# Kernel optimization log

Measured on AMD Instinct MI355X. Metric: run time of the kernel, lower is better.

Reference implementation:

```python
import jax, jax.numpy as jnp
import numpy as np

# db1 (Haar) filters, replicating the torch module's pywt-derived constants.
_s = np.float32(1.0 / np.sqrt(2.0))
_dl = np.array([_s, _s], np.float32)    # dec_lo[::-1]
_dh = np.array([_s, -_s], np.float32)   # dec_hi[::-1]
_rl = np.array([_s, _s], np.float32)    # rec_lo
_rh = np.array([_s, -_s], np.float32)   # rec_hi
# filters[k][i,j] = a[j]*b[i]  (torch: a.unsqueeze(0)*b.unsqueeze(1)) == outer(b, a)
DEC = jnp.asarray(np.stack([np.outer(_dl, _dl) / 2.0, np.outer(_dh, _dl), np.outer(_dl, _dh), np.outer(_dh, _dh)], 0))  # [4,2,2]
REC = jnp.asarray(np.stack([np.outer(_rl, _rl) * 2.0, np.outer(_rh, _rl), np.outer(_rl, _rh), np.outer(_rh, _rh)], 0))  # [4,2,2]


def wt(x):
    # stride-2 2x2 conv per channel == linear mix of 2x2 blocks; fused over all channels
    B, C, H, W = x.shape
    xb = x.reshape(B, C, H // 2, 2, W // 2, 2)
    y = jnp.einsum('kpq,bchpwq->bckhw', DEC, xb)  # [B,C,4,H/2,W/2]
    y = jnp.concatenate([y[:, :, :1], (y[:, :, 1:] + 1.0) * 0.5], axis=2)  # rescale HF bands
    return y.reshape(B, 4 * C, H // 2, W // 2)


def iwt(y):
    B, C4, H, W = y.shape
    C = C4 // 4
    yb = y.reshape(B, C, 4, H, W)
    yb = jnp.concatenate([yb[:, :, :1], 2.0 * yb[:, :, 1:] - 1.0], axis=2)  # undo HF rescale
    x = jnp.einsum('kpq,bckhw->bchpwq', REC, yb)  # conv_transpose2d, stride 2, no overlap
    return x.reshape(B, C, 2 * H, 2 * W)


def conv3x3(x, w, b):
    y = jax.lax.conv_general_dilated(x, w, (1, 1), ((1, 1), (1, 1)), dimension_numbers=('NCHW', 'OIHW', 'NCHW'))
    return y + b[None, :, None, None]


def setup_inputs() -> dict:
    key = jax.random.key(0)
    ks = jax.random.split(key, 20)
    B, Cin, H, W = 8, 1, 512, 512
    c = 16
    inp = {'x': jax.random.normal(ks[0], (B, Cin, H, W), jnp.float32)}
    specs = [('conv1', c, 4 * Cin), ('conv2', 4 * c, 4 * c), ('conv3', 16 * c, 16 * c), ('conv4', 64 * c, 64 * c),
             ('convd1', 4, c), ('convd2', c, 2 * c), ('convd3', 4 * c, 8 * c), ('convd4', 16 * c, 32 * c)]
    for idx, (name, o, i) in enumerate(specs):
        kw, kb = jax.random.split(ks[1 + idx])
        inp[name + '_w'] = jax.random.normal(kw, (o, i, 3, 3), jnp.float32) / np.float32(np.sqrt(i * 9))
        inp[name + '_b'] = jax.random.normal(kb, (o,), jnp.float32) * 0.01
    return inp


def reference(x, conv1_w, conv1_b, conv2_w, conv2_b, conv3_w, conv3_b, conv4_w, conv4_b,
              convd1_w, convd1_b, convd2_w, convd2_b, convd3_w, convd3_b, convd4_w, convd4_b):
    lrelu = lambda t: jax.nn.leaky_relu(t, 0.2)
    w1 = wt(x);  c1 = lrelu(conv3x3(w1, conv1_w, conv1_b))
    w2 = wt(c1); c2 = lrelu(conv3x3(w2, conv2_w, conv2_b))
    w3 = wt(c2); c3 = lrelu(conv3x3(w3, conv3_w, conv3_b))
    w4 = wt(c3); c4 = lrelu(conv3x3(w4, conv4_w, conv4_b))
    c5 = lrelu(conv3x3(c4, conv4_w, conv4_b))  # conv4 reused, as in the torch module
    c6 = conv3x3(c5, conv4_w, conv4_b)
    ic4 = lrelu(c6 + w4)
    ic3 = lrelu(conv3x3(jnp.concatenate([c3, iwt(ic4)], 1), convd4_w, convd4_b))
    ic2 = lrelu(conv3x3(jnp.concatenate([c2, iwt(ic3)], 1), convd3_w, convd3_b))
    ic1 = lrelu(conv3x3(jnp.concatenate([c1, iwt(ic2)], 1), convd2_w, convd2_b))
    iw1 = lrelu(conv3x3(ic1, convd1_w, convd1_b))
    logits = iwt(iw1)
    return jax.nn.sigmoid(logits)
```

## Files before the change

kernel.cpp:

```cpp
#include <hip/hip_runtime.h>
#include <cstddef>


typedef unsigned short u16;
typedef unsigned int u32;
typedef __bf16 bf16x8 __attribute__((ext_vector_type(8)));
typedef float floatx4 __attribute__((ext_vector_type(4)));
typedef u16 u16x4 __attribute__((ext_vector_type(4)));
typedef u16 u16x8 __attribute__((ext_vector_type(8)));

__device__ __forceinline__ float b2f(u16 h) {
    union { u32 u; float f; } x; x.u = ((u32)h) << 16; return x.f;
}
__device__ __forceinline__ u16 f2b(float f) {
    union { float f; u32 u; } x; x.f = f;
    return (u16)((x.u + 0x7FFFu + ((x.u >> 16) & 1u)) >> 16);
}
__device__ __forceinline__ float lrelu_f(float v) { return v > 0.f ? v : 0.2f * v; }

__device__ __forceinline__ void gld16(const u16* g, u16* l) {
    __builtin_amdgcn_global_load_lds(
        (const __attribute__((address_space(1))) u32*)(const void*)g,
        (__attribute__((address_space(3))) u32*)(void*)l, 16, 0, 0);
}

template<int NT>
__global__ __launch_bounds__(256)
void conv_mfma_k(const u16* __restrict__ in, int Cin, int iWp, int iImg,
                 const u16* __restrict__ wb, const float* __restrict__ bias,
                 const u16* __restrict__ skip, int sC, int sWp, int sImg, int spad,
                 u16* __restrict__ out, int Cst, int oWp, int oImg, int opad,
                 int logW, int logH)
{
    constexpr int BM = 128, BN = NT * 32;
    constexpr int ASZ = BM * 32;
    constexpr int BSZ = BN * 32;
    __shared__ u16 At[2 * ASZ];
    __shared__ u16 Bt[2 * BSZ];

    const int tid = threadIdx.x;
    const int wid = tid >> 6, lane = tid & 63;
    const int W = 1 << logW, H = 1 << logH;
    const int mBase = blockIdx.x * BM;
    const int nBase = blockIdx.y * BN;
    const int K = 9 * Cin;
    const int kg = lane & 3;
    const int rr = lane >> 2;
    const int kgs = kg ^ ((rr >> 1) & 3);

    const u16 *gA0, *gA1, *gB0, *gB1 = nullptr;
    {
        int m0 = mBase + wid * 32 + rr;
        int px0 = m0 & (W - 1), py0 = (m0 >> logW) & (H - 1), pb0 = m0 >> (logW + logH);
        gA0 = in + ((size_t)pb0 * iImg + (size_t)py0 * iWp + px0) * Cin + kgs * 8;
        int m1 = m0 + 16;
        int px1 = m1 & (W - 1), py1 = (m1 >> logW) & (H - 1), pb1 = m1 >> (logW + logH);
        gA1 = in + ((size_t)pb1 * iImg + (size_t)py1 * iWp + px1) * Cin + kgs * 8;
    }
    if constexpr (NT == 4) {
        gB0 = wb + (size_t)(nBase + wid * 32 + rr) * K + kgs * 8;
        gB1 = wb + (size_t)(nBase + wid * 32 + 16 + rr) * K + kgs * 8;
    } else {
        gB0 = wb + (size_t)(nBase + wid * 16 + rr) * K + kgs * 8;
    }
    u16* lA0 = &At[wid * 1024];
    u16* lA1 = &At[wid * 1024 + 512];
    u16* lB0 = (NT == 4) ? &Bt[wid * 1024] : &Bt[wid * 512];
    u16* lB1 = (NT == 4) ? &Bt[wid * 1024 + 512] : nullptr;

    const int wm = wid >> 1, wn = wid & 1;
    const int fm = lane & 15;
    const int fk = ((lane >> 4) * 8) ^ (((fm >> 1) & 3) << 3);

    floatx4 acc[4][NT] = {};

    const int nChunks = K / 32;
    const size_t rowStep = (size_t)(iWp - 2) * Cin;
    int cbn = 0, tap = 0;

    auto stage = [&](int buf) {
        gld16(gA0, lA0 + buf * ASZ);
        gld16(gA1, lA1 + buf * ASZ);
        gld16(gB0, lB0 + buf * BSZ);
        if constexpr (NT == 4) gld16(gB1, lB1 + buf * BSZ);
        size_t dA = 32;
        cbn += 32;
        if (cbn == Cin) { cbn = 0; ++tap; dA = ((tap % 3 == 0) ? rowStep : (size_t)Cin) - (size_t)(Cin - 32); }
        gA0 += dA; gA1 += dA;
        gB0 += 32;
        if constexpr (NT == 4) gB1 += 32;
    };

    auto compute = [&](int buf) {
        const u16* Ab = &At[buf * ASZ];
        const u16* Bb = &Bt[buf * BSZ];
        bf16x8 af[4], bfr[NT];
#pragma unroll
        for (int mt = 0; mt < 4; ++mt)
            af[mt] = *(const bf16x8*)&Ab[(wm * 64 + mt * 16 + fm) * 32 + fk];
#pragma unroll
        for (int nt = 0; nt < NT; ++nt)
            bfr[nt] = *(const bf16x8*)&Bb[(wn * (NT * 16) + nt * 16 + fm) * 32 + fk];
        __builtin_amdgcn_s_setprio(1);
#pragma unroll
        for (int mt = 0; mt < 4; ++mt)
#pragma unroll
            for (int nt = 0; nt < NT; ++nt)
                acc[mt][nt] = __builtin_amdgcn_mfma_f32_16x16x32_bf16(af[mt], bfr[nt], acc[mt][nt], 0, 0, 0);
        __builtin_amdgcn_s_setprio(0);
    };

    stage(0);
    __syncthreads();
    for (int kc = 0; kc < nChunks; kc += 2) {
        stage(1);
        compute(0);
        __syncthreads();
        if (kc + 2 < nChunks) stage(0);
        compute(1);
        __syncthreads();
    }

    const int rq = (lane >> 4) * 4;
#pragma unroll
    for (int mt = 0; mt < 4; ++mt) {
        const int mrow = mBase + wm * 64 + mt * 16 + rq;
#pragma unroll
        for (int r = 0; r < 4; ++r) {
            int m2 = mrow + r;
            int px = m2 & (W - 1), py = (m2 >> logW) & (H - 1), pb = m2 >> (logW + logH);
            size_t ob = ((size_t)pb * oImg + (size_t)(py + opad) * oWp + (px + opad)) * Cst;
            size_t sb = 0;
            if (skip) sb = ((size_t)pb * sImg + (size_t)(py + spad) * sWp + (px + spad)) * sC;
#pragma unroll
            for (int nt = 0; nt < NT; ++nt) {
                int n = nBase + wn * (NT * 16) + nt * 16 + fm;
                float v = acc[mt][nt][r] + bias[n];
                if (skip) v += b2f(skip[sb + n]);
                v = lrelu_f(v);
                out[ob + n] = f2b(v);
            }
        }
    }
}

__global__ __launch_bounds__(256)
void conv_n16_k(const u16* __restrict__ in, int iWp, int iImg,
                const u16* __restrict__ wb, const float* __restrict__ bias,
                u16* __restrict__ out, int logW, int logH)
{
    __shared__ u16 At[128 * 32];
    __shared__ u16 Bt[16 * 32];
    const int tid = threadIdx.x;
    const int wid = tid >> 6, lane = tid & 63;
    const int W = 1 << logW, H = 1 << logH;
    const int mBase = blockIdx.x * 128;
    const int kg = lane & 3, rr = lane >> 2;
    const int kgs = kg ^ ((rr >> 1) & 3);

    const u16 *gA0, *gA1;
    {
        int m0 = mBase + wid * 32 + rr;
        int px0 = m0 & (W - 1), py0 = (m0 >> logW) & (H - 1), pb0 = m0 >> (logW + logH);
        gA0 = in + ((size_t)pb0 * iImg + (size_t)py0 * iWp + px0) * 32 + kgs * 8;
        int m1 = m0 + 16;
        int px1 = m1 & (W - 1), py1 = (m1 >> logW) & (H - 1), pb1 = m1 >> (logW + logH);
        gA1 = in + ((size_t)pb1 * iImg + (size_t)py1 * iWp + px1) * 32 + kgs * 8;
    }
    const u16* gB = wb + (size_t)rr * 288 + kgs * 8;
    u16* lA0 = &At[wid * 1024];
    u16* lA1 = &At[wid * 1024 + 512];

    const int fm = lane & 15;
    const int fk = ((lane >> 4) * 8) ^ (((fm >> 1) & 3) << 3);
    floatx4 acc[2] = {};
    const size_t rowStep = (size_t)(iWp - 2) * 32;

    for (int tap = 0; tap < 9; ++tap) {
        gld16(gA0, lA0);
        gld16(gA1, lA1);
        if (wid == 0) gld16(gB, &Bt[0]);
        __syncthreads();
        bf16x8 bf = *(const bf16x8*)&Bt[fm * 32 + fk];
#pragma unroll
        for (int mt = 0; mt < 2; ++mt) {
            bf16x8 af = *(const bf16x8*)&At[(wid * 32 + mt * 16 + fm) * 32 + fk];
            acc[mt] = __builtin_amdgcn_mfma_f32_16x16x32_bf16(af, bf, acc[mt], 0, 0, 0);
        }
        __syncthreads();
        size_t dA = (tap % 3 == 2) ? rowStep : (size_t)32;
        gA0 += dA; gA1 += dA; gB += 32;
    }

    const int rq = (lane >> 4) * 4;
    const float bn = bias[fm];
#pragma unroll
    for (int mt = 0; mt < 2; ++mt) {
#pragma unroll
        for (int r = 0; r < 4; ++r) {
            int m2 = mBase + wid * 32 + mt * 16 + rq + r;
            out[(size_t)m2 * 16 + fm] = f2b(lrelu_f(acc[mt][r] + bn));
        }
    }
}

template<int CIN, int COUT>
__global__ __launch_bounds__(256)
void conv_direct_k(const u16* __restrict__ in, int Sin,
                   const float* __restrict__ w, const float* __restrict__ bias,
                   u16* __restrict__ out, int Sout, int oWp, int oImg, int opad,
                   int logW, int logH, int total)
{
    int m = blockIdx.x * 256 + threadIdx.x;
    if (m >= total) return;
    const int W = 1 << logW, H = 1 << logH;
    const int px = m & (W - 1);
    const int py = (m >> logW) & (H - 1);
    const int pb = m >> (logW + logH);
    float acc[COUT];
#pragma unroll
    for (int o = 0; o < COUT; ++o) acc[o] = bias[o];
    for (int tap = 0; tap < 9; ++tap) {
        int dy = tap / 3 - 1, dx = tap % 3 - 1;
        int iy = py + dy, ix = px + dx;
        if ((unsigned)iy >= (unsigned)H || (unsigned)ix >= (unsigned)W) continue;
        const u16* p = in + (size_t)((((pb << logH) + iy) << logW) + ix) * Sin;
        if constexpr (CIN == 4) {
            u16x4 v = *(const u16x4*)p;
#pragma unroll
            for (int ci = 0; ci < 4; ++ci) {
                float f = b2f(v[ci]);
#pragma unroll
                for (int o = 0; o < COUT; ++o) acc[o] += f * w[(o * CIN + ci) * 9 + tap];
            }
        } else {
#pragma unroll
            for (int c8 = 0; c8 < CIN / 8; ++c8) {
                u16x8 v = *(const u16x8*)(p + c8 * 8);
#pragma unroll
                for (int j = 0; j < 8; ++j) {
                    int ci = c8 * 8 + j;
                    float f = b2f(v[j]);
#pragma unroll
                    for (int o = 0; o < COUT; ++o) acc[o] += f * w[(o * CIN + ci) * 9 + tap];
                }
            }
        }
    }
    size_t ob = ((size_t)pb * oImg + (size_t)(py + opad) * oWp + (px + opad)) * Sout;
#pragma unroll
    for (int o = 0; o < COUT; ++o)
        out[ob + o] = f2b(lrelu_f(acc[o]));
}

__global__ __launch_bounds__(256)
void wt_in_k(const float* __restrict__ x, u16* __restrict__ out, int total)
{
    int idx = blockIdx.x * 256 + threadIdx.x;
    if (idx >= total) return;
    int wq = idx & 255, t = idx >> 8;
    int hq = t & 255, b = t >> 8;
    const float* p = x + ((size_t)b * 512 + 2 * hq) * 512 + 2 * wq;
    float a = p[0], bv = p[1], cv = p[512], d = p[513];
    u16x4 o = { f2b(0.25f * (a + bv + cv + d)),
                f2b(0.25f * (a + bv - cv - d) + 0.5f),
                f2b(0.25f * (a - bv + cv - d) + 0.5f),
                f2b(0.25f * (a - bv - cv + d) + 0.5f) };
    *(u16x4*)&out[(size_t)idx * 4] = o;
}

__global__ __launch_bounds__(256)
void wt_k(const u16* __restrict__ in, int Sin, int iWp, int iImg, int ipad,
          u16* __restrict__ out, int Sout, int oWp, int oImg, int opad,
          int logC, int logWo, int logHo, int total)
{
    int idx = blockIdx.x * 256 + threadIdx.x;
    if (idx >= total) return;
    const int C = 1 << logC, Wo = 1 << logWo, Ho = 1 << logHo;
    int c = idx & (C - 1); int t = idx >> logC;
    int wq = t & (Wo - 1); t >>= logWo;
    int hq = t & (Ho - 1); int b = t >> logHo;
    size_t p00 = ((size_t)b * iImg + (size_t)(2 * hq + ipad) * iWp + (2 * wq + ipad)) * Sin + c;
    float a  = b2f(in[p00]);
    float bv = b2f(in[p00 + Sin]);
    float cv = b2f(in[p00 + (size_t)iWp * Sin]);
    float d  = b2f(in[p00 + (size_t)iWp * Sin + Sin]);
    u16x4 o = { f2b(0.25f * (a + bv + cv + d)),
                f2b(0.25f * (a + bv - cv - d) + 0.5f),
                f2b(0.25f * (a - bv + cv - d) + 0.5f),
                f2b(0.25f * (a - bv - cv + d) + 0.5f) };
    *(u16x4*)&out[((size_t)b * oImg + (size_t)(hq + opad) * oWp + (wq + opad)) * Sout + 4 * c] = o;
}

__global__ __launch_bounds__(256)
void iwt_k(const u16* __restrict__ in, int Sin, int logC, int logW, int logH,
           u16* __restrict__ out, int Sout, int oWp, int oImg, int opad, int total)
{
    int idx = blockIdx.x * 256 + threadIdx.x;
    if (idx >= total) return;
    const int C = 1 << logC, W = 1 << logW;
    int c = idx & (C - 1); int t = idx >> logC;
    int wq = t & (W - 1); t >>= logW;
    int hq = t & ((1 << logH) - 1); int b = t >> logH;
    u16x4 v = *(const u16x4*)&in[(size_t)((((b << logH) + hq) << logW) + wq) * Sin + 4 * c];
    float y0 = b2f(v[0]);
    float y1 = 2.f * b2f(v[1]) - 1.f;
    float y2 = 2.f * b2f(v[2]) - 1.f;
    float y3 = 2.f * b2f(v[3]) - 1.f;
    float x00 = y0 + 0.5f * ( y1 + y2 + y3);
    float x01 = y0 + 0.5f * ( y1 - y2 - y3);
    float x10 = y0 + 0.5f * (-y1 + y2 - y3);
    float x11 = y0 + 0.5f * (-y1 - y2 + y3);
    size_t q = ((size_t)b * oImg + (size_t)(2 * hq + opad) * oWp + (2 * wq + opad)) * Sout + c;
    out[q] = f2b(x00);
    out[q + Sout] = f2b(x01);
    out[q + (size_t)oWp * Sout] = f2b(x10);
    out[q + (size_t)oWp * Sout + Sout] = f2b(x11);
}

__global__ __launch_bounds__(256)
void iwt_out_k(const u16* __restrict__ in, float* __restrict__ out, int total)
{
    int idx = blockIdx.x * 256 + threadIdx.x;
    if (idx >= total) return;
    int wq = idx & 255, t = idx >> 8;
    int hq = t & 255, b = t >> 8;
    u16x4 v = *(const u16x4*)&in[(size_t)idx * 4];
    float y0 = b2f(v[0]);
    float y1 = 2.f * b2f(v[1]) - 1.f;
    float y2 = 2.f * b2f(v[2]) - 1.f;
    float y3 = 2.f * b2f(v[3]) - 1.f;
    float x00 = y0 + 0.5f * ( y1 + y2 + y3);
    float x01 = y0 + 0.5f * ( y1 - y2 - y3);
    float x10 = y0 + 0.5f * (-y1 + y2 - y3);
    float x11 = y0 + 0.5f * (-y1 - y2 + y3);
    float* q = out + ((size_t)b * 512 + 2 * hq) * 512 + 2 * wq;
    q[0]   = 1.f / (1.f + __expf(-x00));
    q[1]   = 1.f / (1.f + __expf(-x01));
    q[512] = 1.f / (1.f + __expf(-x10));
    q[513] = 1.f / (1.f + __expf(-x11));
}

__global__ __launch_bounds__(256)
void prep_w_k(const float* __restrict__ src, u16* __restrict__ dst, int logCIN, int total)
{
    int idx = blockIdx.x * 256 + threadIdx.x;
    if (idx >= total) return;
    const int CIN = 1 << logCIN;
    int ci = idx & (CIN - 1);
    int q = idx >> logCIN;
    int tap = q % 9, o = q / 9;
    dst[idx] = f2b(src[((size_t)(o * CIN + ci)) * 9 + tap]);
}

__global__ __launch_bounds__(256)
void zb_k(u16* __restrict__ buf, int Wp, int Hp, int C, int total)
{
    int idx = blockIdx.x * 256 + threadIdx.x;
    if (idx >= total) return;
    int c8 = idx % (C / 8); int t = idx / (C / 8);
    int nbp = 2 * Wp + 2 * (Hp - 2);
    int p = t % nbp; int b = t / nbp;
    int y, x;
    if (p < Wp) { y = 0; x = p; }
    else if (p < 2 * Wp) { y = Hp - 1; x = p - Wp; }
    else { int q = p - 2 * Wp; y = 1 + (q >> 1); x = (q & 1) ? Wp - 1 : 0; }
    u16x8 z = {0, 0, 0, 0, 0, 0, 0, 0};
    *(u16x8*)&buf[((size_t)b * Hp * Wp + (size_t)y * Wp + x) * C + c8 * 8] = z;
}

extern "C" void kernel_launch(void* const* d_in, const int* in_sizes, int n_in,
                              void* d_out, int out_size, void* d_ws, size_t ws_size,
                              hipStream_t stream)
{
    const float* x   = (const float*)d_in[0];
    const float* c1w = (const float*)d_in[1];  const float* c1b = (const float*)d_in[2];
    const float* c2w = (const float*)d_in[3];  const float* c2b = (const float*)d_in[4];
    const float* c3w = (const float*)d_in[5];  const float* c3b = (const float*)d_in[6];
    const float* c4w = (const float*)d_in[7];  const float* c4b = (const float*)d_in[8];
    const float* d1w = (const float*)d_in[9];  const float* d1b = (const float*)d_in[10];
    const float* d2w = (const float*)d_in[11]; const float* d2b = (const float*)d_in[12];
    const float* d3w = (const float*)d_in[13]; const float* d3b = (const float*)d_in[14];
    const float* d4w = (const float*)d_in[15]; const float* d4b = (const float*)d_in[16];

    const size_t MiB = 1u << 20;
    char* base = (char*)d_ws;
    u16* c4wb = (u16*)base;
    u16* c3wb = c4wb + 9437184;
    u16* d4wb = c3wb + 589824;
    u16* d3wb = d4wb + 1179648;
    u16* c2wb = d3wb + 73728;
    u16* d2wb = c2wb + 36864;
    u16* CAT1p = (u16*)(base + 22  * MiB);
    u16* CAT2p = (u16*)(base + 55  * MiB);
    u16* CAT3p = (u16*)(base + 88  * MiB);
    u16* P1    = (u16*)(base + 123 * MiB);
    u16* P2    = (u16*)(base + 142 * MiB);
    u16* P3    = (u16*)(base + 161 * MiB);
    float* outp = (float*)d_out;

    u16* W2p = P1; u16* W4p = P1; u16* IC2 = P1;
    u16* W3p = P2; u16* C4p = P2; u16* IC4 = P2; u16* IC1 = P2;
    u16* W1  = P3; u16* C5p = P3; u16* IC3 = P3; u16* IW1 = P3;

    auto cdiv = [](int a, int b) { return (a + b - 1) / b; };
    auto prep = [&](const float* s, u16* d, int logCIN, int total) {
        prep_w_k<<<cdiv(total, 256), 256, 0, stream>>>(s, d, logCIN, total);
    };
    auto zb = [&](u16* buf, int Wp, int Hp, int C) {
        int total = 8 * (2 * Wp + 2 * (Hp - 2)) * (C / 8);
        zb_k<<<cdiv(total, 256), 256, 0, stream>>>(buf, Wp, Hp, C, total);
    };
    auto mfma = [&](const u16* in, int Cin, int iWp, int iImg,
                    const u16* w, const float* bi,
                    const u16* skip, int sC, int sWp, int sImg, int spad,
                    int Cout, u16* out, int Cst, int oWp, int oImg, int opad,
                    int logW, int logH) {
        int M = 8 << (logW + logH);
        if (Cout % 128 == 0) {
            dim3 g(M / 128, Cout / 128);
            conv_mfma_k<4><<<g, 256, 0, stream>>>(in, Cin, iWp, iImg, w, bi,
                                                  skip, sC, sWp, sImg, spad,
                                                  out, Cst, oWp, oImg, opad, logW, logH);
        } else {
            dim3 g(M / 128, Cout / 64);
            conv_mfma_k<2><<<g, 256, 0, stream>>>(in, Cin, iWp, iImg, w, bi,
                                                  skip, sC, sWp, sImg, spad,
                                                  out, Cst, oWp, oImg, opad, logW, logH);
        }
    };

    prep(c4w, c4wb, 10, 9437184);
    prep(c3w, c3wb, 8, 589824);
    prep(d4w, d4wb, 9, 1179648);
    prep(d3w, d3wb, 7, 73728);
    prep(c2w, c2wb, 6, 36864);
    prep(d2w, d2wb, 5, 4608);
    zb(CAT1p, 258, 258, 32);
    zb(W2p, 130, 130, 64);
    zb(W3p, 66, 66, 256);
    zb(CAT2p, 130, 130, 128);
    zb(CAT3p, 66, 66, 512);

    const int P256 = 8 * 256 * 256;
    const int T2M = 2097152;
    const int I258 = 258 * 258;

    wt_in_k<<<cdiv(P256, 256), 256, 0, stream>>>(x, W1, P256);
    conv_direct_k<4, 16><<<cdiv(P256, 256), 256, 0, stream>>>(
        W1, 4, c1w, c1b, CAT1p, 32, 258, I258, 1, 8, 8, P256);
    zb(C5p, 34, 34, 1024);
    wt_k<<<cdiv(T2M, 256), 256, 0, stream>>>(CAT1p, 32, 258, I258, 1,
                                             W2p, 64, 130, 16900, 1, 4, 7, 7, T2M);
    mfma(W2p, 64, 130, 16900, c2wb, c2b, nullptr, 0, 0, 0, 0,
         64, CAT2p, 128, 130, 16900, 1, 7, 7);
    zb(W4p, 34, 34, 1024);
    wt_k<<<cdiv(T2M, 256), 256, 0, stream>>>(CAT2p, 128, 130, 16900, 1,
                                             W3p, 256, 66, 4356, 1, 6, 6, 6, T2M);
    mfma(W3p, 256, 66, 4356, c3wb, c3b, nullptr, 0, 0, 0, 0,
         256, CAT3p, 512, 66, 4356, 1, 6, 6);
    zb(C4p, 34, 34, 1024);
    wt_k<<<cdiv(T2M, 256), 256, 0, stream>>>(CAT3p, 512, 66, 4356, 1,
                                             W4p, 1024, 34, 1156, 1, 8, 5, 5, T2M);
    mfma(W4p, 1024, 34, 1156, c4wb, c4b, nullptr, 0, 0, 0, 0,
         1024, C4p, 1024, 34, 1156, 1, 5, 5);
    mfma(C4p, 1024, 34, 1156, c4wb, c4b, nullptr, 0, 0, 0, 0,
         1024, C5p, 1024, 34, 1156, 1, 5, 5);
    mfma(C5p, 1024, 34, 1156, c4wb, c4b, W4p, 1024, 34, 1156, 1,
         1024, IC4, 1024, 32, 1024, 0, 5, 5);
    iwt_k<<<cdiv(T2M, 256), 256, 0, stream>>>(IC4, 1024, 8, 5, 5,
                                              CAT3p + 256, 512, 66, 4356, 1, T2M);
    mfma(CAT3p, 512, 66, 4356, d4wb, d4b, nullptr, 0, 0, 0, 0,
         256, IC3, 256, 64, 4096, 0, 6, 6);
    iwt_k<<<cdiv(T2M, 256), 256, 0, stream>>>(IC3, 256, 6, 6, 6,
                                              CAT2p + 64, 128, 130, 16900, 1, T2M);
    mfma(CAT2p, 128, 130, 16900, d3wb, d3b, nullptr, 0, 0, 0, 0,
         64, IC2, 64, 128, 16384, 0, 7, 7);
    iwt_k<<<cdiv(T2M, 256), 256, 0, stream>>>(IC2, 64, 4, 7, 7,
                                              CAT1p + 16, 32, 258, I258, 1, T2M);
    conv_n16_k<<<dim3(P256 / 128), 256, 0, stream>>>(CAT1p, 258, I258, d2wb, d2b, IC1, 8, 8);
    conv_direct_k<16, 4><<<cdiv(P256, 256), 256, 0, stream>>>(
        IC1, 16, d1w, d1b, IW1, 4, 256, 65536, 0, 8, 8, P256);
    iwt_out_k<<<cdiv(P256, 256), 256, 0, stream>>>(IW1, outp, P256);
}
```

Measured before the change: 1.034 ms.

## Load MFMA B fragments directly from pre-tiled weights, dropping B LDS staging

Weights are pre-permuted into a fragment-ordered tiled layout so each lane can read its MFMA B operand straight from global memory into registers with one 16-byte load per tile. The B shared-memory buffer and its async LDS copies are removed, and B fragments are double-buffered in registers. Block indices are also remapped so blocks sharing an M tile run adjacently across N, which should improve cache reuse of activations. The change trades LDS traffic and capacity for more global/L2 weight reads per wave, which may expose latency.

```diff
diff --git a/kernel.cpp b/kernel.cpp
--- a/kernel.cpp
+++ b/kernel.cpp
@@ -34,21 +34,24 @@
 {
     constexpr int BM = 128, BN = NT * 32;
     constexpr int ASZ = BM * 32;
-    constexpr int BSZ = BN * 32;
     __shared__ u16 At[2 * ASZ];
-    __shared__ u16 Bt[2 * BSZ];
 
     const int tid = threadIdx.x;
     const int wid = tid >> 6, lane = tid & 63;
     const int W = 1 << logW, H = 1 << logH;
-    const int mBase = blockIdx.x * BM;
-    const int nBase = blockIdx.y * BN;
+
+    const int id = blockIdx.x + gridDim.x * blockIdx.y;
+    const int by = id % gridDim.y;
+    const int bx = id / gridDim.y;
+    const int mBase = bx * BM;
+    const int nBase = by * BN;
+
     const int K = 9 * Cin;
     const int kg = lane & 3;
     const int rr = lane >> 2;
     const int kgs = kg ^ ((rr >> 1) & 3);
 
-    const u16 *gA0, *gA1, *gB0, *gB1 = nullptr;
+    const u16 *gA0, *gA1;
     {
         int m0 = mBase + wid * 32 + rr;
         int px0 = m0 & (W - 1), py0 = (m0 >> logW) & (H - 1), pb0 = m0 >> (logW + logH);
@@ -57,50 +60,45 @@
         int px1 = m1 & (W - 1), py1 = (m1 >> logW) & (H - 1), pb1 = m1 >> (logW + logH);
         gA1 = in + ((size_t)pb1 * iImg + (size_t)py1 * iWp + px1) * Cin + kgs * 8;
     }
-    if constexpr (NT == 4) {
-        gB0 = wb + (size_t)(nBase + wid * 32 + rr) * K + kgs * 8;
-        gB1 = wb + (size_t)(nBase + wid * 32 + 16 + rr) * K + kgs * 8;
-    } else {
-        gB0 = wb + (size_t)(nBase + wid * 16 + rr) * K + kgs * 8;
-    }
     u16* lA0 = &At[wid * 1024];
     u16* lA1 = &At[wid * 1024 + 512];
-    u16* lB0 = (NT == 4) ? &Bt[wid * 1024] : &Bt[wid * 512];
-    u16* lB1 = (NT == 4) ? &Bt[wid * 1024 + 512] : nullptr;
 
     const int wm = wid >> 1, wn = wid & 1;
     const int fm = lane & 15;
     const int fk = ((lane >> 4) * 8) ^ (((fm >> 1) & 3) << 3);
 
+    const int nG = gridDim.y * (NT * 2);
+    const size_t bStride = (size_t)nG * 512;
+    const u16* gBbase = wb + (size_t)((nBase >> 4) + wn * NT) * 512 + lane * 8;
+
     floatx4 acc[4][NT] = {};
 
     const int nChunks = K / 32;
     const size_t rowStep = (size_t)(iWp - 2) * Cin;
     int cbn = 0, tap = 0;
 
-    auto stage = [&](int buf) {
+    auto stageA = [&](int buf) {
         gld16(gA0, lA0 + buf * ASZ);
         gld16(gA1, lA1 + buf * ASZ);
-        gld16(gB0, lB0 + buf * BSZ);
-        if constexpr (NT == 4) gld16(gB1, lB1 + buf * BSZ);
         size_t dA = 32;
         cbn += 32;
         if (cbn == Cin) { cbn = 0; ++tap; dA = ((tap % 3 == 0) ? rowStep : (size_t)Cin) - (size_t)(Cin - 32); }
         gA0 += dA; gA1 += dA;
-        gB0 += 32;
-        if constexpr (NT == 4) gB1 += 32;
     };
 
-    auto compute = [&](int buf) {
+    auto loadB = [&](bf16x8 (&dst)[NT], int kc) {
+        const u16* p = gBbase + (size_t)kc * bStride;
+#pragma unroll
+        for (int nt = 0; nt < NT; ++nt)
+            dst[nt] = *(const bf16x8*)(p + nt * 512);
+    };
+
+    auto compute = [&](int buf, const bf16x8 (&bfr)[NT]) {
         const u16* Ab = &At[buf * ASZ];
-        const u16* Bb = &Bt[buf * BSZ];
-        bf16x8 af[4], bfr[NT];
+        bf16x8 af[4];
 #pragma unroll
         for (int mt = 0; mt < 4; ++mt)
             af[mt] = *(const bf16x8*)&Ab[(wm * 64 + mt * 16 + fm) * 32 + fk];
-#pragma unroll
-        for (int nt = 0; nt < NT; ++nt)
-            bfr[nt] = *(const bf16x8*)&Bb[(wn * (NT * 16) + nt * 16 + fm) * 32 + fk];
         __builtin_amdgcn_s_setprio(1);
 #pragma unroll
         for (int mt = 0; mt < 4; ++mt)
@@ -110,14 +108,16 @@
         __builtin_amdgcn_s_setprio(0);
     };
 
-    stage(0);
+    bf16x8 bC[NT], bN[NT];
+    stageA(0); loadB(bC, 0);
     __syncthreads();
     for (int kc = 0; kc < nChunks; kc += 2) {
-        stage(1);
-        compute(0);
+        stageA(1);
+        loadB(bN, kc + 1);
+        compute(0, bC);
         __syncthreads();
-        if (kc + 2 < nChunks) stage(0);
-        compute(1);
+        if (kc + 2 < nChunks) { stageA(0); loadB(bC, kc + 2); }
+        compute(1, bN);
         __syncthreads();
     }
 
@@ -354,6 +354,25 @@
 }
 
 __global__ __launch_bounds__(256)
+void prep_w_tiled_k(const float* __restrict__ src, u16* __restrict__ dst,
+                    int logCIN, int logNG, int total)
+{
+    int idx = blockIdx.x * 256 + threadIdx.x;
+    if (idx >= total) return;
+    const int CIN = 1 << logCIN;
+    int j = idx & 7;
+    int r = (idx >> 3) & 15;
+    int q = (idx >> 7) & 3;
+    int t = idx >> 9;
+    int g = t & ((1 << logNG) - 1);
+    int kc = t >> logNG;
+    int o = g * 16 + r;
+    int k = kc * 32 + q * 8 + j;
+    int tap = k >> logCIN, ci = k & (CIN - 1);
+    dst[idx] = f2b(src[((size_t)o * CIN + ci) * 9 + tap]);
+}
+
+__global__ __launch_bounds__(256)
 void zb_k(u16* __restrict__ buf, int Wp, int Hp, int C, int total)
 {
     int idx = blockIdx.x * 256 + threadIdx.x;
@@ -404,8 +423,8 @@
     u16* W1  = P3; u16* C5p = P3; u16* IC3 = P3; u16* IW1 = P3;
 
     auto cdiv = [](int a, int b) { return (a + b - 1) / b; };
-    auto prep = [&](const float* s, u16* d, int logCIN, int total) {
-        prep_w_k<<<cdiv(total, 256), 256, 0, stream>>>(s, d, logCIN, total);
+    auto prepT = [&](const float* s, u16* d, int logCIN, int logNG, int total) {
+        prep_w_tiled_k<<<cdiv(total, 256), 256, 0, stream>>>(s, d, logCIN, logNG, total);
     };
     auto zb = [&](u16* buf, int Wp, int Hp, int C) {
         int total = 8 * (2 * Wp + 2 * (Hp - 2)) * (C / 8);
@@ -430,12 +449,12 @@
         }
     };
 
-    prep(c4w, c4wb, 10, 9437184);
-    prep(c3w, c3wb, 8, 589824);
-    prep(d4w, d4wb, 9, 1179648);
-    prep(d3w, d3wb, 7, 73728);
-    prep(c2w, c2wb, 6, 36864);
-    prep(d2w, d2wb, 5, 4608);
+    prepT(c4w, c4wb, 10, 6, 9437184);
+    prepT(c3w, c3wb, 8, 4, 589824);
+    prepT(d4w, d4wb, 9, 4, 1179648);
+    prepT(d3w, d3wb, 7, 2, 73728);
+    prepT(c2w, c2wb, 6, 2, 36864);
+    prep_w_k<<<cdiv(4608, 256), 256, 0, stream>>>(d2w, d2wb, 5, 4608);
     zb(CAT1p, 258, 258, 32);
     zb(W2p, 130, 130, 64);
     zb(W3p, 66, 66, 256);
```

New measurement: 1.179 ms. +14.0%, slower.

## Triple-buffer MFMA conv LDS staging with partial vmcnt waits

Applied to the files above, without the earlier changes.

Replaces the double-buffered K-loop with a three-stage LDS ring, keeping two chunks of global-to-LDS loads in flight while one is computed. Each iteration ends with a hand-written s_waitcnt vmcnt(N) plus barrier that waits only for the oldest stage's loads instead of draining all outstanding loads. The goal is to hide global memory latency better. In exchange it uses 1.5x more shared memory per block, which may reduce occupancy, and the hard-coded vmcnt values must match the number of loads each stage issues.

```diff
diff --git a/kernel.cpp b/kernel.cpp
--- a/kernel.cpp
+++ b/kernel.cpp
@@ -35,8 +35,8 @@
     constexpr int BM = 128, BN = NT * 32;
     constexpr int ASZ = BM * 32;
     constexpr int BSZ = BN * 32;
-    __shared__ u16 At[2 * ASZ];
-    __shared__ u16 Bt[2 * BSZ];
+    __shared__ u16 At[3 * ASZ];
+    __shared__ u16 Bt[3 * BSZ];
 
     const int tid = threadIdx.x;
     const int wid = tid >> 6, lane = tid & 63;
@@ -110,15 +110,27 @@
         __builtin_amdgcn_s_setprio(0);
     };
 
+    auto waitbar = [&](bool partial) {
+        if (partial) {
+            if constexpr (NT == 4) asm volatile("s_waitcnt vmcnt(4)\ns_barrier" ::: "memory");
+            else                   asm volatile("s_waitcnt vmcnt(3)\ns_barrier" ::: "memory");
+        } else {
+            asm volatile("s_waitcnt vmcnt(0)\ns_barrier" ::: "memory");
+        }
+    };
+
     stage(0);
-    __syncthreads();
-    for (int kc = 0; kc < nChunks; kc += 2) {
-        stage(1);
-        compute(0);
-        __syncthreads();
-        if (kc + 2 < nChunks) stage(0);
-        compute(1);
-        __syncthreads();
+    stage(1);
+    waitbar(true);
+
+    int cb = 0, pb = 2;
+    for (int kc = 0; kc < nChunks; ++kc) {
+        bool pre = (kc + 2 < nChunks);
+        if (pre) stage(pb);
+        compute(cb);
+        waitbar(pre);
+        pb = cb;
+        cb = (cb == 2) ? 0 : cb + 1;
     }
 
     const int rq = (lane >> 4) * 4;
@@ -128,10 +140,10 @@
 #pragma unroll
         for (int r = 0; r < 4; ++r) {
             int m2 = mrow + r;
-            int px = m2 & (W - 1), py = (m2 >> logW) & (H - 1), pb = m2 >> (logW + logH);
-            size_t ob = ((size_t)pb * oImg + (size_t)(py + opad) * oWp + (px + opad)) * Cst;
+            int px = m2 & (W - 1), py = (m2 >> logW) & (H - 1), pb2 = m2 >> (logW + logH);
+            size_t ob = ((size_t)pb2 * oImg + (size_t)(py + opad) * oWp + (px + opad)) * Cst;
             size_t sb = 0;
-            if (skip) sb = ((size_t)pb * sImg + (size_t)(py + spad) * sWp + (px + spad)) * sC;
+            if (skip) sb = ((size_t)pb2 * sImg + (size_t)(py + spad) * sWp + (px + spad)) * sC;
 #pragma unroll
             for (int nt = 0; nt < NT; ++nt) {
                 int n = nBase + wn * (NT * 16) + nt * 16 + fm;
```

Measured after the change: 1.086 ms. 5.0% more time.

## Split K across two wave groups in 512-thread conv kernel with LDS reduction

Applied to the files above, without the earlier changes.

Adds a 512-thread conv kernel for Cout%128 layers. Two groups of four waves each handle half of the K reduction, using separate double-buffered LDS regions. At the end the partial accumulators are summed through LDS before the fused bias/skip/lrelu epilogue. The goal is more waves per 128x128 tile, to hide latency on the deep-K layers, especially conv4 at small spatial size. In exchange it costs extra LDS traffic and a sync for the reduction. It also assumes nChunks splits evenly into even halves.

```diff
diff --git a/kernel.cpp b/kernel.cpp
--- a/kernel.cpp
+++ b/kernel.cpp
@@ -24,7 +24,146 @@
         (__attribute__((address_space(3))) u32*)(void*)l, 16, 0, 0);
 }
 
-template<int NT>
+__global__ __launch_bounds__(512, 4)
+void conv_mfma8_k(const u16* __restrict__ in, int Cin, int iWp, int iImg,
+                  const u16* __restrict__ wb, const float* __restrict__ bias,
+                  const u16* __restrict__ skip, int sC, int sWp, int sImg, int spad,
+                  u16* __restrict__ out, int Cst, int oWp, int oImg, int opad,
+                  int logW, int logH)
+{
+    __shared__ alignas(16) u16 S[32768];
+
+    const int tid = threadIdx.x;
+    const int wid = tid >> 6, lane = tid & 63;
+    const int half = wid >> 2, wl = wid & 3;
+    const int W = 1 << logW, H = 1 << logH;
+    const int mBase = blockIdx.x * 128;
+    const int nBase = blockIdx.y * 128;
+    const int K = 9 * Cin;
+    const int nChunks = K / 32;
+    const int nC = nChunks >> 1;
+
+    const int kg = lane & 3;
+    const int rr = lane >> 2;
+    const int kgs = kg ^ ((rr >> 1) & 3);
+
+    const int k0 = half * nC * 32;
+    int tap = k0 / Cin;
+    int cbn = k0 - tap * Cin;
+
+    const u16 *gA0, *gA1, *gB0, *gB1;
+    {
+        int ty = tap / 3, tx = tap - ty * 3;
+        int m0 = mBase + wl * 32 + rr;
+        int px0 = m0 & (W - 1), py0 = (m0 >> logW) & (H - 1), pb0 = m0 >> (logW + logH);
+        gA0 = in + ((size_t)pb0 * iImg + (size_t)(py0 + ty) * iWp + (px0 + tx)) * Cin + cbn + kgs * 8;
+        int m1 = m0 + 16;
+        int px1 = m1 & (W - 1), py1 = (m1 >> logW) & (H - 1), pb1 = m1 >> (logW + logH);
+        gA1 = in + ((size_t)pb1 * iImg + (size_t)(py1 + ty) * iWp + (px1 + tx)) * Cin + cbn + kgs * 8;
+    }
+    gB0 = wb + (size_t)(nBase + wl * 32 + rr) * K + k0 + kgs * 8;
+    gB1 = wb + (size_t)(nBase + wl * 32 + 16 + rr) * K + k0 + kgs * 8;
+
+    u16* Sb = &S[half * 16384];
+    u16* lA0 = Sb + wl * 1024;
+    u16* lA1 = Sb + wl * 1024 + 512;
+    u16* lB0 = Sb + 8192 + wl * 1024;
+    u16* lB1 = Sb + 8192 + wl * 1024 + 512;
+
+    const int wm = wl >> 1, wn = wl & 1;
+    const int fm = lane & 15;
+    const int fk = ((lane >> 4) * 8) ^ (((fm >> 1) & 3) << 3);
+
+    floatx4 acc[4][4] = {};
+
+    const size_t rowStep = (size_t)(iWp - 2) * Cin;
+
+    auto stage = [&](int buf) {
+        gld16(gA0, lA0 + buf * 4096);
+        gld16(gA1, lA1 + buf * 4096);
+        gld16(gB0, lB0 + buf * 4096);
+        gld16(gB1, lB1 + buf * 4096);
+        size_t dA = 32;
+        cbn += 32;
+        if (cbn == Cin) { cbn = 0; ++tap; dA = ((tap % 3 == 0) ? rowStep : (size_t)Cin) - (size_t)(Cin - 32); }
+        gA0 += dA; gA1 += dA;
+        gB0 += 32; gB1 += 32;
+    };
+
+    auto compute = [&](int buf) {
+        const u16* Ab = Sb + buf * 4096;
+        const u16* Bb = Sb + 8192 + buf * 4096;
+        bf16x8 af[4], bfr[4];
+#pragma unroll
+        for (int mt = 0; mt < 4; ++mt)
+            af[mt] = *(const bf16x8*)&Ab[(wm * 64 + mt * 16 + fm) * 32 + fk];
+#pragma unroll
+        for (int nt = 0; nt < 4; ++nt)
+            bfr[nt] = *(const bf16x8*)&Bb[(wn * 64 + nt * 16 + fm) * 32 + fk];
+        __builtin_amdgcn_s_setprio(1);
+#pragma unroll
+        for (int mt = 0; mt < 4; ++mt)
+#pragma unroll
+            for (int nt = 0; nt < 4; ++nt)
+                acc[mt][nt] = __builtin_amdgcn_mfma_f32_16x16x32_bf16(af[mt], bfr[nt], acc[mt][nt], 0, 0, 0);
+        __builtin_amdgcn_s_setprio(0);
+    };
+
+    stage(0);
+    __syncthreads();
+    for (int kc = 0; kc < nC; kc += 2) {
+        stage(1);
+        compute(0);
+        __syncthreads();
+        if (kc + 2 < nC) stage(0);
+        compute(1);
+        __syncthreads();
+    }
+
+    float* R = (float*)S;
+    if (half == 1) {
+#pragma unroll
+        for (int mt = 0; mt < 4; ++mt)
+#pragma unroll
+            for (int nt = 0; nt < 4; ++nt) {
+                int j = mt * 4 + nt;
+                *(floatx4*)&R[(size_t)(((wl * 16 + j) * 64) + lane) * 4] = acc[mt][nt];
+            }
+    }
+    __syncthreads();
+    if (half == 0) {
+        const int rq = (lane >> 4) * 4;
+#pragma unroll
+        for (int mt = 0; mt < 4; ++mt)
+#pragma unroll
+            for (int nt = 0; nt < 4; ++nt) {
+                int j = mt * 4 + nt;
+                floatx4 v = *(const floatx4*)&R[(size_t)(((wl * 16 + j) * 64) + lane) * 4];
+                acc[mt][nt] = acc[mt][nt] + v;
+            }
+#pragma unroll
+        for (int mt = 0; mt < 4; ++mt) {
+            const int mrow = mBase + wm * 64 + mt * 16 + rq;
+#pragma unroll
+            for (int r = 0; r < 4; ++r) {
+                int m2 = mrow + r;
+                int px = m2 & (W - 1), py = (m2 >> logW) & (H - 1), pb2 = m2 >> (logW + logH);
+                size_t ob = ((size_t)pb2 * oImg + (size_t)(py + opad) * oWp + (px + opad)) * Cst;
+                size_t sb = 0;
+                if (skip) sb = ((size_t)pb2 * sImg + (size_t)(py + spad) * sWp + (px + spad)) * sC;
+#pragma unroll
+                for (int nt = 0; nt < 4; ++nt) {
+                    int n = nBase + wn * 64 + nt * 16 + fm;
+                    float v = acc[mt][nt][r] + bias[n];
+                    if (skip) v += b2f(skip[sb + n]);
+                    v = lrelu_f(v);
+                    out[ob + n] = f2b(v);
+                }
+            }
+        }
+    }
+}
+
 __global__ __launch_bounds__(256)
 void conv_mfma_k(const u16* __restrict__ in, int Cin, int iWp, int iImg,
                  const u16* __restrict__ wb, const float* __restrict__ bias,
@@ -32,6 +171,7 @@
                  u16* __restrict__ out, int Cst, int oWp, int oImg, int opad,
                  int logW, int logH)
 {
+    constexpr int NT = 2;
     constexpr int BM = 128, BN = NT * 32;
     constexpr int ASZ = BM * 32;
     constexpr int BSZ = BN * 32;
@@ -48,7 +188,7 @@
     const int rr = lane >> 2;
     const int kgs = kg ^ ((rr >> 1) & 3);
 
-    const u16 *gA0, *gA1, *gB0, *gB1 = nullptr;
+    const u16 *gA0, *gA1, *gB0;
     {
         int m0 = mBase + wid * 32 + rr;
         int px0 = m0 & (W - 1), py0 = (m0 >> logW) & (H - 1), pb0 = m0 >> (logW + logH);
@@ -57,16 +197,10 @@
         int px1 = m1 & (W - 1), py1 = (m1 >> logW) & (H - 1), pb1 = m1 >> (logW + logH);
         gA1 = in + ((size_t)pb1 * iImg + (size_t)py1 * iWp + px1) * Cin + kgs * 8;
     }
-    if constexpr (NT == 4) {
-        gB0 = wb + (size_t)(nBase + wid * 32 + rr) * K + kgs * 8;
-        gB1 = wb + (size_t)(nBase + wid * 32 + 16 + rr) * K + kgs * 8;
-    } else {
-        gB0 = wb + (size_t)(nBase + wid * 16 + rr) * K + kgs * 8;
-    }
+    gB0 = wb + (size_t)(nBase + wid * 16 + rr) * K + kgs * 8;
     u16* lA0 = &At[wid * 1024];
     u16* lA1 = &At[wid * 1024 + 512];
-    u16* lB0 = (NT == 4) ? &Bt[wid * 1024] : &Bt[wid * 512];
-    u16* lB1 = (NT == 4) ? &Bt[wid * 1024 + 512] : nullptr;
+    u16* lB0 = &Bt[wid * 512];
 
     const int wm = wid >> 1, wn = wid & 1;
     const int fm = lane & 15;
@@ -82,13 +216,11 @@
         gld16(gA0, lA0 + buf * ASZ);
         gld16(gA1, lA1 + buf * ASZ);
         gld16(gB0, lB0 + buf * BSZ);
-        if constexpr (NT == 4) gld16(gB1, lB1 + buf * BSZ);
         size_t dA = 32;
         cbn += 32;
         if (cbn == Cin) { cbn = 0; ++tap; dA = ((tap % 3 == 0) ? rowStep : (size_t)Cin) - (size_t)(Cin - 32); }
         gA0 += dA; gA1 += dA;
         gB0 += 32;
-        if constexpr (NT == 4) gB1 += 32;
     };
 
     auto compute = [&](int buf) {
@@ -128,10 +260,10 @@
 #pragma unroll
         for (int r = 0; r < 4; ++r) {
             int m2 = mrow + r;
-            int px = m2 & (W - 1), py = (m2 >> logW) & (H - 1), pb = m2 >> (logW + logH);
-            size_t ob = ((size_t)pb * oImg + (size_t)(py + opad) * oWp + (px + opad)) * Cst;
+            int px = m2 & (W - 1), py = (m2 >> logW) & (H - 1), pb2 = m2 >> (logW + logH);
+            size_t ob = ((size_t)pb2 * oImg + (size_t)(py + opad) * oWp + (px + opad)) * Cst;
             size_t sb = 0;
-            if (skip) sb = ((size_t)pb * sImg + (size_t)(py + spad) * sWp + (px + spad)) * sC;
+            if (skip) sb = ((size_t)pb2 * sImg + (size_t)(py + spad) * sWp + (px + spad)) * sC;
 #pragma unroll
             for (int nt = 0; nt < NT; ++nt) {
                 int n = nBase + wn * (NT * 16) + nt * 16 + fm;
@@ -419,14 +551,14 @@
         int M = 8 << (logW + logH);
         if (Cout % 128 == 0) {
             dim3 g(M / 128, Cout / 128);
-            conv_mfma_k<4><<<g, 256, 0, stream>>>(in, Cin, iWp, iImg, w, bi,
-                                                  skip, sC, sWp, sImg, spad,
-                                                  out, Cst, oWp, oImg, opad, logW, logH);
+            conv_mfma8_k<<<g, 512, 0, stream>>>(in, Cin, iWp, iImg, w, bi,
+                                                skip, sC, sWp, sImg, spad,
+                                                out, Cst, oWp, oImg, opad, logW, logH);
         } else {
             dim3 g(M / 128, Cout / 64);
-            conv_mfma_k<2><<<g, 256, 0, stream>>>(in, Cin, iWp, iImg, w, bi,
-                                                  skip, sC, sWp, sImg, spad,
-                                                  out, Cst, oWp, oImg, opad, logW, logH);
+            conv_mfma_k<<<g, 256, 0, stream>>>(in, Cin, iWp, iImg, w, bi,
+                                               skip, sC, sWp, sImg, spad,
+                                               out, Cst, oWp, oImg, opad, logW, logH);
         }
     };
 
```

After: 1.009 ms. -2.5%, faster.
